# Kernel tuning notes

Measured on AMD Instinct MI355X. Metric: run time of the kernel, lower is better.

Reference implementation:

```python
import jax, jax.numpy as jnp
import numpy as np

N = 8192
IN_F = 512
OUT_F = 64
NEG_SLOPE = 0.01  # nn.LeakyReLU default
MASK_VAL = -1e9


def setup_inputs() -> dict:
    key = jax.random.key(0)
    k_h, k_adj, k_W, k_a = jax.random.split(key, 4)
    h = jax.random.normal(k_h, (N, IN_F), dtype=jnp.float32)
    adjacency = jax.random.randint(k_adj, (N, N), 0, 2, dtype=jnp.int32)
    # xavier_uniform bounds
    bW = float(np.sqrt(6.0 / (IN_F + OUT_F)))
    ba = float(np.sqrt(6.0 / (2 * OUT_F + 1)))
    W = jax.random.uniform(k_W, (IN_F, OUT_F), minval=-bW, maxval=bW, dtype=jnp.float32)
    a = jax.random.uniform(k_a, (2 * OUT_F, 1), minval=-ba, maxval=ba, dtype=jnp.float32)
    return {"h": h, "adjacency": adjacency, "W": W, "a": a}


def reference(h, adjacency, W, a):
    WH = h @ W                                  # [N, out_f]
    wh1 = WH @ a[:OUT_F, :]                     # [N, 1]
    wh2 = WH @ a[OUT_F:, :]                     # [N, 1]
    e = jax.nn.leaky_relu(wh1 + wh2.T, negative_slope=NEG_SLOPE)  # [N, N]
    attnt = jnp.where(adjacency > 0, e, jnp.float32(MASK_VAL))
    attnt = jax.nn.softmax(attnt, axis=1)       # row-wise softmax
    hfirst = attnt @ WH                         # [N, out_f]
    return jax.nn.elu(hfirst)
```

## Files before the change

### kernel.cpp

```cpp
#include <hip/hip_runtime.h>
#include <hip/hip_bf16.h>

#define N 8192
#define IN_F 512
#define OUT_F 64
#define S_SPLIT 16
#define JT (N / S_SPLIT)

typedef __attribute__((ext_vector_type(8))) short short8;
typedef __attribute__((ext_vector_type(4))) float floatx4;
typedef __attribute__((ext_vector_type(4))) int intx4;

__device__ inline short f2bf(float x) {
    __hip_bfloat16 b = __float2bfloat16(x);
    return __builtin_bit_cast(short, b);
}

__global__ void k_wt(const float* __restrict__ W, short* __restrict__ WT) {
    int idx = blockIdx.x * 256 + threadIdx.x;
    int k = idx >> 6, f = idx & 63;
    WT[f * IN_F + k] = f2bf(W[k * OUT_F + f]);
}

__global__ __launch_bounds__(64) void k_wh(const float* __restrict__ h,
                                           const short* __restrict__ WT,
                                           float* __restrict__ WH,
                                           short* __restrict__ WHbT) {
    __shared__ float tile[OUT_F][17];
    int lane = threadIdx.x;
    int n = lane & 15, q = lane >> 4;
    int i0 = blockIdx.x * 16;
    int rowA = i0 + n;
    const float* hp = h + (size_t)rowA * IN_F + q * 8;
    floatx4 acc[4] = {};
    for (int k0 = 0; k0 < IN_F; k0 += 32) {
        floatx4 h0 = *(const floatx4*)(hp + k0);
        floatx4 h1 = *(const floatx4*)(hp + k0 + 4);
        short8 af;
#pragma unroll
        for (int j = 0; j < 4; j++) { af[j] = f2bf(h0[j]); af[j + 4] = f2bf(h1[j]); }
#pragma unroll
        for (int b = 0; b < 4; b++) {
            short8 bf_ = *(const short8*)(WT + (b * 16 + n) * IN_F + k0 + q * 8);
            acc[b] = __builtin_amdgcn_mfma_f32_16x16x32_bf16(af, bf_, acc[b], 0, 0, 0);
        }
    }
#pragma unroll
    for (int b = 0; b < 4; b++) {
#pragma unroll
        for (int r = 0; r < 4; r++) {
            int rl = q * 4 + r;
            int col = b * 16 + n;
            float v = acc[b][r];
            WH[(i0 + rl) * OUT_F + col] = v;
            tile[col][rl] = v;
        }
    }
    __syncthreads();
    const float* tc = tile[lane];
    short8 s0, s1;
#pragma unroll
    for (int k = 0; k < 8; k++) { s0[k] = f2bf(tc[k]); s1[k] = f2bf(tc[k + 8]); }
    *(short8*)(WHbT + (size_t)lane * N + i0) = s0;
    *(short8*)(WHbT + (size_t)lane * N + i0 + 8) = s1;
}

__global__ void k_wh12(const float* __restrict__ WH, const float* __restrict__ a,
                       float* __restrict__ wh1, float* __restrict__ wh2) {
    int row = blockIdx.x * 256 + threadIdx.x;
    float s1 = 0.f, s2 = 0.f;
#pragma unroll 8
    for (int f = 0; f < OUT_F; f++) {
        float v = WH[row * OUT_F + f];
        s1 += v * a[f];
        s2 += v * a[OUT_F + f];
    }
    wh1[row] = s1;
    wh2[row] = s2;
}

__global__ __launch_bounds__(256, 6) void k_attn(const int* __restrict__ adj,
                                                 const short* __restrict__ WHbT,
                                                 const float* __restrict__ wh1,
                                                 const float* __restrict__ wh2,
                                                 float* __restrict__ num_part,
                                                 float* __restrict__ den_part) {
    int w = threadIdx.x >> 6;
    int lane = threadIdx.x & 63;
    int n = lane & 15, q = lane >> 4;
    int i0 = blockIdx.x * 64 + w * 16;
    int rowA = i0 + n;
    int split = blockIdx.y;
    int j0 = split * JT;

    const int* ap = adj + (size_t)rowA * N + j0 + q * 8;
    const float* w2p = wh2 + j0 + q * 8;
    const short* bp0 = WHbT + (size_t)n * N + j0 + q * 8;
    float my_wh1 = wh1[rowA];

    floatx4 acc[4] = {};
    float dsum = 0.f;

    intx4 ca0 = *(const intx4*)(ap);
    intx4 ca1 = *(const intx4*)(ap + 4);
    floatx4 cw0 = *(const floatx4*)(w2p);
    floatx4 cw1 = *(const floatx4*)(w2p + 4);

    for (int t = 0; t < JT; t += 32) {
        intx4 na0 = ca0, na1 = ca1;
        floatx4 nw0 = cw0, nw1 = cw1;
        if (t + 32 < JT) {
            na0 = *(const intx4*)(ap + 32);
            na1 = *(const intx4*)(ap + 36);
            nw0 = *(const floatx4*)(w2p + 32);
            nw1 = *(const floatx4*)(w2p + 36);
        }
        short8 bfr[4];
#pragma unroll
        for (int b = 0; b < 4; b++)
            bfr[b] = *(const short8*)(bp0 + (size_t)b * 16 * N + t);

        float p[8];
#pragma unroll
        for (int jj = 0; jj < 8; jj++) {
            int av = (jj < 4) ? ca0[jj] : ca1[jj - 4];
            float e = my_wh1 + ((jj < 4) ? cw0[jj] : cw1[jj - 4]);
            float el = fmaxf(e, 0.01f * e);
            float pv = __expf(el);
            pv = (av > 0) ? pv : 0.f;
            p[jj] = pv;
            dsum += pv;
        }
        short8 af;
#pragma unroll
        for (int jj = 0; jj < 8; jj++) af[jj] = f2bf(p[jj]);
#pragma unroll
        for (int b = 0; b < 4; b++)
            acc[b] = __builtin_amdgcn_mfma_f32_16x16x32_bf16(af, bfr[b], acc[b], 0, 0, 0);

        ap += 32; w2p += 32;
        ca0 = na0; ca1 = na1; cw0 = nw0; cw1 = nw1;
    }

    dsum += __shfl_xor(dsum, 16, 64);
    dsum += __shfl_xor(dsum, 32, 64);
    if (q == 0) den_part[(size_t)split * N + rowA] = dsum;

    float* np_ = num_part + (size_t)split * N * OUT_F;
#pragma unroll
    for (int b = 0; b < 4; b++)
#pragma unroll
        for (int r = 0; r < 4; r++)
            np_[(i0 + q * 4 + r) * OUT_F + b * 16 + n] = acc[b][r];
}

__global__ void k_final(const float* __restrict__ num_part,
                        const float* __restrict__ den_part,
                        float* __restrict__ out) {
    int idx = blockIdx.x * 256 + threadIdx.x;
    int row = idx >> 6;
    float s = 0.f, d = 0.f;
#pragma unroll
    for (int sp = 0; sp < S_SPLIT; sp++) {
        s += num_part[(size_t)sp * N * OUT_F + idx];
        d += den_part[sp * N + row];
    }
    float x = s / d;
    out[idx] = (x > 0.f) ? x : (__expf(x) - 1.f);
}

extern "C" void kernel_launch(void* const* d_in, const int* in_sizes, int n_in,
                              void* d_out, int out_size, void* d_ws, size_t ws_size,
                              hipStream_t stream) {
    const float* h = (const float*)d_in[0];
    const int* adj = (const int*)d_in[1];
    const float* W = (const float*)d_in[2];
    const float* a = (const float*)d_in[3];
    float* out = (float*)d_out;

    char* ws = (char*)d_ws;
    float* WH    = (float*)(ws);
    short* WHbT  = (short*)(ws + (size_t)(2 << 20));
    short* WT    = (short*)(ws + (size_t)(3 << 20));
    float* wh1   = (float*)(ws + (size_t)(3 << 20) + (64 << 10));
    float* wh2   = wh1 + N;
    float* num_p = (float*)(ws + (size_t)(4 << 20));
    float* den_p = (float*)(ws + (size_t)(36 << 20));

    k_wt<<<dim3(128), dim3(256), 0, stream>>>(W, WT);
    k_wh<<<dim3(N / 16), dim3(64), 0, stream>>>(h, WT, WH, WHbT);
    k_wh12<<<dim3(N / 256), dim3(256), 0, stream>>>(WH, a, wh1, wh2);
    k_attn<<<dim3(128, S_SPLIT), dim3(256), 0, stream>>>(adj, WHbT, wh1, wh2, num_p, den_p);
    k_final<<<dim3((N * OUT_F) / 256), dim3(256), 0, stream>>>(num_p, den_p, out);
}
```

Measured before the change: 444.5 us.

## Pack adjacency into bitmask in a pre-pass and read bits in attention kernel

Adds a kernel that compresses the int32 adjacency matrix into a bitmask (one bit per edge). The attention kernel then loads 64 bytes of mask per row segment up front instead of streaming int32 adjacency values, and fully unrolls its loop. The adjacency still has to be read once by the pack pass, but the attention kernel's memory traffic and register pressure from the adjacency loads go down. The launch-bounds occupancy hint drops from 6 to 4, and an extra kernel launch plus a mask write are added.

```diff
diff --git a/kernel.cpp b/kernel.cpp
--- a/kernel.cpp
+++ b/kernel.cpp
@@ -6,6 +6,7 @@
 #define OUT_F 64
 #define S_SPLIT 16
 #define JT (N / S_SPLIT)
+#define NB (N / 8)
 
 typedef __attribute__((ext_vector_type(8))) short short8;
 typedef __attribute__((ext_vector_type(4))) float floatx4;
@@ -14,6 +15,21 @@
 __device__ inline short f2bf(float x) {
     __hip_bfloat16 b = __float2bfloat16(x);
     return __builtin_bit_cast(short, b);
+}
+
+__global__ __launch_bounds__(256) void k_pack(const int* __restrict__ adj,
+                                              unsigned* __restrict__ mask) {
+    int t = blockIdx.x * 256 + threadIdx.x;
+    const int* p = adj + (size_t)t * 32;
+    unsigned b = 0;
+#pragma unroll
+    for (int c = 0; c < 8; c++) {
+        intx4 v = *(const intx4*)(p + c * 4);
+#pragma unroll
+        for (int j = 0; j < 4; j++)
+            b |= (v[j] > 0 ? 1u : 0u) << (c * 4 + j);
+    }
+    mask[t] = b;
 }
 
 __global__ void k_wt(const float* __restrict__ W, short* __restrict__ WT) {
@@ -79,7 +95,7 @@
     wh2[row] = s2;
 }
 
-__global__ __launch_bounds__(256, 6) void k_attn(const int* __restrict__ adj,
+__global__ __launch_bounds__(256, 4) void k_attn(const unsigned char* __restrict__ mask,
                                                  const short* __restrict__ WHbT,
                                                  const float* __restrict__ wh1,
                                                  const float* __restrict__ wh2,
@@ -93,41 +109,35 @@
     int split = blockIdx.y;
     int j0 = split * JT;
 
-    const int* ap = adj + (size_t)rowA * N + j0 + q * 8;
+    const intx4* mp = (const intx4*)(mask + (size_t)rowA * NB + (j0 >> 3));
+    intx4 mdw0 = mp[0], mdw1 = mp[1], mdw2 = mp[2], mdw3 = mp[3];
+
     const float* w2p = wh2 + j0 + q * 8;
     const short* bp0 = WHbT + (size_t)n * N + j0 + q * 8;
     float my_wh1 = wh1[rowA];
 
     floatx4 acc[4] = {};
     float dsum = 0.f;
-
-    intx4 ca0 = *(const intx4*)(ap);
-    intx4 ca1 = *(const intx4*)(ap + 4);
-    floatx4 cw0 = *(const floatx4*)(w2p);
-    floatx4 cw1 = *(const floatx4*)(w2p + 4);
-
-    for (int t = 0; t < JT; t += 32) {
-        intx4 na0 = ca0, na1 = ca1;
-        floatx4 nw0 = cw0, nw1 = cw1;
-        if (t + 32 < JT) {
-            na0 = *(const intx4*)(ap + 32);
-            na1 = *(const intx4*)(ap + 36);
-            nw0 = *(const floatx4*)(w2p + 32);
-            nw1 = *(const floatx4*)(w2p + 36);
-        }
+    int qs = q * 8;
+
+#pragma unroll
+    for (int s = 0; s < 16; s++) {
+        unsigned md = (unsigned)((s < 4) ? mdw0[s] : (s < 8) ? mdw1[s - 4]
+                               : (s < 12) ? mdw2[s - 8] : mdw3[s - 12]);
+        floatx4 w20 = *(const floatx4*)(w2p + s * 32);
+        floatx4 w21 = *(const floatx4*)(w2p + s * 32 + 4);
         short8 bfr[4];
 #pragma unroll
         for (int b = 0; b < 4; b++)
-            bfr[b] = *(const short8*)(bp0 + (size_t)b * 16 * N + t);
+            bfr[b] = *(const short8*)(bp0 + (size_t)b * 16 * N + s * 32);
 
         float p[8];
 #pragma unroll
         for (int jj = 0; jj < 8; jj++) {
-            int av = (jj < 4) ? ca0[jj] : ca1[jj - 4];
-            float e = my_wh1 + ((jj < 4) ? cw0[jj] : cw1[jj - 4]);
+            float e = my_wh1 + ((jj < 4) ? w20[jj] : w21[jj - 4]);
             float el = fmaxf(e, 0.01f * e);
             float pv = __expf(el);
-            pv = (av > 0) ? pv : 0.f;
+            pv = ((md >> (qs + jj)) & 1u) ? pv : 0.f;
             p[jj] = pv;
             dsum += pv;
         }
@@ -137,9 +147,6 @@
 #pragma unroll
         for (int b = 0; b < 4; b++)
             acc[b] = __builtin_amdgcn_mfma_f32_16x16x32_bf16(af, bfr[b], acc[b], 0, 0, 0);
-
-        ap += 32; w2p += 32;
-        ca0 = na0; ca1 = na1; cw0 = nw0; cw1 = nw1;
     }
 
     dsum += __shfl_xor(dsum, 16, 64);
@@ -179,17 +186,20 @@
     float* out = (float*)d_out;
 
     char* ws = (char*)d_ws;
-    float* WH    = (float*)(ws);
-    short* WHbT  = (short*)(ws + (size_t)(2 << 20));
-    short* WT    = (short*)(ws + (size_t)(3 << 20));
-    float* wh1   = (float*)(ws + (size_t)(3 << 20) + (64 << 10));
-    float* wh2   = wh1 + N;
-    float* num_p = (float*)(ws + (size_t)(4 << 20));
-    float* den_p = (float*)(ws + (size_t)(36 << 20));
-
+    float* WH       = (float*)(ws);
+    short* WHbT     = (short*)(ws + (size_t)(2 << 20));
+    short* WT       = (short*)(ws + (size_t)(3 << 20));
+    float* wh1      = (float*)(ws + (size_t)(3 << 20) + (64 << 10));
+    float* wh2      = wh1 + N;
+    unsigned* maskb = (unsigned*)(ws + (size_t)(4 << 20));
+    float* num_p    = (float*)(ws + (size_t)(16 << 20));
+    float* den_p    = (float*)(ws + (size_t)(48 << 20));
+
+    k_pack<<<dim3((N / 8 * N / 4) / 256), dim3(256), 0, stream>>>(adj, maskb);
     k_wt<<<dim3(128), dim3(256), 0, stream>>>(W, WT);
     k_wh<<<dim3(N / 16), dim3(64), 0, stream>>>(h, WT, WH, WHbT);
     k_wh12<<<dim3(N / 256), dim3(256), 0, stream>>>(WH, a, wh1, wh2);
-    k_attn<<<dim3(128, S_SPLIT), dim3(256), 0, stream>>>(adj, WHbT, wh1, wh2, num_p, den_p);
+    k_attn<<<dim3(128, S_SPLIT), dim3(256), 0, stream>>>((const unsigned char*)maskb,
+                                                         WHbT, wh1, wh2, num_p, den_p);
     k_final<<<dim3((N * OUT_F) / 256), dim3(256), 0, stream>>>(num_p, den_p, out);
 }
```

Result: slower. 460.8 us (+3.7%).
